# Performance work log

Hardware: AMD Instinct MI355X
Metric: run time of the kernel (lower is better)

## Reference

```python
import jax, jax.numpy as jnp
import numpy as np

T, BATCH, DMODEL, H = 2048, 16, 512, 512


def setup_inputs() -> dict:
    key = jax.random.key(0)
    ks = jax.random.split(key, 8)
    x = jax.random.normal(ks[0], (T, BATCH, DMODEL), jnp.float32)
    # initial carry: (lambda=1, h=0) so the concat trick leaves state untouched
    h0_re = jnp.zeros((1, BATCH, H), jnp.float32)
    h0_im = jnp.zeros((1, BATCH, H), jnp.float32)
    # LRU parameterization (Orvieto et al. 2023): |lambda| in [0.9, 0.99]
    u1 = jax.random.uniform(ks[1], (H,), jnp.float32)
    nu_log = jnp.log(-0.5 * jnp.log(u1 * (0.99 ** 2 - 0.9 ** 2) + 0.9 ** 2))
    theta_log = jnp.log(jax.random.uniform(ks[2], (H,), jnp.float32) * (np.pi / 10) + 1e-4)
    B_re = jax.random.normal(ks[3], (H, DMODEL), jnp.float32) / np.sqrt(2 * DMODEL)
    B_im = jax.random.normal(ks[4], (H, DMODEL), jnp.float32) / np.sqrt(2 * DMODEL)
    C_re = jax.random.normal(ks[5], (DMODEL, H), jnp.float32) / np.sqrt(H)
    C_im = jax.random.normal(ks[6], (DMODEL, H), jnp.float32) / np.sqrt(H)
    D_vec = jax.random.normal(ks[7], (DMODEL,), jnp.float32)
    return dict(x=x, h0_re=h0_re, h0_im=h0_im, nu_log=nu_log, theta_log=theta_log,
                B_re=B_re, B_im=B_im, C_re=C_re, C_im=C_im, D_vec=D_vec)


def _binop(qi, qj):
    # associative combine for h_t = a_t * h_{t-1} + b_t
    a_i, b_i = qi
    a_j, b_j = qj
    return (a_j * a_i, a_j * b_i + b_j)


def reference(x, h0_re, h0_im, nu_log, theta_log, B_re, B_im, C_re, C_im, D_vec):
    # diagonal complex recurrence eigenvalues, |Lambda| = exp(-exp(nu_log)) < 1
    Lam = jnp.exp(-jnp.exp(nu_log) + 1j * jnp.exp(theta_log))        # [H] complex64
    gamma = jnp.sqrt(1.0 - jnp.exp(-2.0 * jnp.exp(nu_log)))           # [H]
    Bmat = (B_re + 1j * B_im) * gamma[:, None]                         # [H, D]
    # map_to_h: Bu elements and broadcast Lambda elements
    Bu = jnp.einsum('tbd,hd->tbh', x.astype(jnp.complex64), Bmat)      # [T, B, H]
    Lam_el = jnp.broadcast_to(Lam, Bu.shape)                            # [T, B, H]
    # concat previous state (lambda=1, b=h0) as first scan element
    h0 = (h0_re + 1j * h0_im).astype(jnp.complex64)                    # [1, B, H]
    a = jnp.concatenate([jnp.ones_like(h0), Lam_el], axis=0)          # [T+1, B, H]
    b = jnp.concatenate([h0, Bu], axis=0)                              # [T+1, B, H]
    _, h_all = jax.lax.associative_scan(_binop, (a, b), axis=0)
    h = h_all[1:]                                                       # [T, B, H]
    # map_from_h: y = Re(C h) + D * x (elementwise skip)
    Cmat = C_re + 1j * C_im                                             # [D, H]
    y = jnp.einsum('tbh,dh->tbd', h, Cmat).real + D_vec * x            # [T, B, D]
    final_state = h[-1:]                                                # [1, B, H]
    return (final_state, y)
```

## Files before the change

kernel.cpp:

```cpp
#include <hip/hip_runtime.h>
#include <hip/hip_bf16.h>
#include <stdint.h>

typedef short shortx8 __attribute__((ext_vector_type(8)));
typedef float floatx4 __attribute__((ext_vector_type(4)));

#define T_LEN 2048
#define BATCH 16
#define DMODEL 512
#define HDIM 512
#define M_ROWS (T_LEN * BATCH)
#define NCHUNK 64
#define LCHUNK 32
#define NCHAIN (BATCH * HDIM)
#define Y_ELEMS (M_ROWS * DMODEL)

__device__ __forceinline__ unsigned short f2bf(float f) {
    union { float f; unsigned u; } v; v.f = f;
    unsigned r = (v.u + 0x7FFFu + ((v.u >> 16) & 1u)) >> 16;
    return (unsigned short)r;
}
__device__ __forceinline__ float bf2f(unsigned short u) {
    union { unsigned u; float f; } v; v.u = ((unsigned)u) << 16;
    return v.f;
}
__device__ __forceinline__ unsigned pk2(float a, float b) {
    union { __hip_bfloat162 h; unsigned u; } v;
    v.h = __float22bfloat162_rn(make_float2(a, b));
    return v.u;
}

__global__ void prep_kernel(const float* __restrict__ nu_log, const float* __restrict__ th_log,
                            float* lam_re, float* lam_im, float* l32_re, float* l32_im, float* gam) {
    int h = blockIdx.x * blockDim.x + threadIdx.x;
    if (h >= HDIM) return;
    double nu  = exp((double)nu_log[h]);
    double th  = exp((double)th_log[h]);
    double mag = exp(-nu);
    double lre = mag * cos(th), lim = mag * sin(th);
    double g   = sqrt(1.0 - exp(-2.0 * nu));
    double zr = lre, zi = lim;
    for (int i = 0; i < 5; ++i) { double nr = zr*zr - zi*zi; zi = 2.0*zr*zi; zr = nr; }
    lam_re[h] = (float)lre; lam_im[h] = (float)lim;
    l32_re[h] = (float)zr;  l32_im[h] = (float)zi;
    gam[h] = (float)g;
}

__global__ void conv_BC_kernel(const float* __restrict__ B_re, const float* __restrict__ B_im,
                               const float* __restrict__ gam,
                               const float* __restrict__ C_re, const float* __restrict__ C_im,
                               unsigned short* __restrict__ Bs, unsigned short* __restrict__ C2) {
    int idx = blockIdx.x * blockDim.x + threadIdx.x;
    if (idx < 524288) {
        int n = idx >> 9;
        int d = idx & 511;
        int h = n >> 1, pb = n & 1;
        float v = (pb ? B_im[h * DMODEL + d] : B_re[h * DMODEL + d]) * gam[h];
        Bs[idx] = f2bf(v);
    } else {
        int i2 = idx - 524288;
        int d = i2 >> 10;
        int k = i2 & 1023;
        int h = k >> 1, pb = k & 1;
        float v = pb ? -C_im[d * HDIM + h] : C_re[d * HDIM + h];
        C2[i2] = f2bf(v);
    }
}

__global__ __launch_bounds__(256, 4) void gemm_xb(const float* __restrict__ X,
                                                  const unsigned short* __restrict__ Bmat,
                                                  unsigned short* __restrict__ Out) {
    const int K = 512, N = 1024, lgNB = 3;
    __shared__ unsigned short As[128 * 64];
    __shared__ unsigned short Bsh[128 * 64];
    const int L = blockIdx.x;
    const int xcd = L & 7;
    const int slot = L >> 3;
    const int bn = slot & ((1 << lgNB) - 1);
    const int bm = xcd * 32 + (slot >> lgNB);
    const int tid = threadIdx.x;
    const int wv = tid >> 6, lane = tid & 63;
    const int wr = wv >> 1, wc = wv & 1;
    const int lrow = lane & 15, qq = lane >> 4;
    floatx4 acc[4][4] = {};

    const size_t rowA = (size_t)bm * 128, rowB = (size_t)bn * 128;
    for (int k0 = 0; k0 < K; k0 += 64) {
        #pragma unroll
        for (int j = 0; j < 4; ++j) {
            int ch  = j * 256 + wv * 64 + lane;
            int r   = ch >> 3;
            int c16 = ch & 7;
            int g16 = c16 ^ (r & 7);
            const unsigned short* gb = Bmat + (rowB + r) * (size_t)K + (k0 + g16 * 8);
            unsigned short* lb = Bsh + (size_t)(j * 256 + wv * 64) * 8;
            __builtin_amdgcn_global_load_lds((const __attribute__((address_space(1))) void*)gb,
                                             (__attribute__((address_space(3))) void*)lb, 16, 0, 0);
        }
        #pragma unroll
        for (int j = 0; j < 4; ++j) {
            int ch  = j * 256 + tid;
            int r   = ch >> 3;
            int c16 = ch & 7;
            int g16 = c16 ^ (r & 7);
            const float* gx = X + (rowA + r) * (size_t)K + (k0 + g16 * 8);
            float4 a0 = *(const float4*)gx;
            float4 a1 = *(const float4*)(gx + 4);
            uint4 w;
            w.x = pk2(a0.x, a0.y); w.y = pk2(a0.z, a0.w);
            w.z = pk2(a1.x, a1.y); w.w = pk2(a1.z, a1.w);
            *(uint4*)&As[(size_t)ch * 8] = w;
        }
        __syncthreads();
        #pragma unroll
        for (int s = 0; s < 2; ++s) {
            shortx8 af[4], bf[4];
            #pragma unroll
            for (int mi = 0; mi < 4; ++mi) {
                int row = wr * 64 + mi * 16 + lrow;
                int c16 = (s * 4 + qq) ^ (row & 7);
                af[mi] = *(const shortx8*)&As[row * 64 + c16 * 8];
            }
            #pragma unroll
            for (int ni = 0; ni < 4; ++ni) {
                int row = wc * 64 + ni * 16 + lrow;
                int c16 = (s * 4 + qq) ^ (row & 7);
                bf[ni] = *(const shortx8*)&Bsh[row * 64 + c16 * 8];
            }
            #pragma unroll
            for (int mi = 0; mi < 4; ++mi)
                #pragma unroll
                for (int ni = 0; ni < 4; ++ni)
                    acc[mi][ni] = __builtin_amdgcn_mfma_f32_16x16x32_bf16(af[mi], bf[ni], acc[mi][ni], 0, 0, 0);
        }
        __syncthreads();
    }
    #pragma unroll
    for (int mi = 0; mi < 4; ++mi) {
        int mbase = bm * 128 + wr * 64 + mi * 16 + qq * 4;
        #pragma unroll
        for (int ni = 0; ni < 4; ++ni) {
            int n = bn * 128 + wc * 64 + ni * 16 + lrow;
            #pragma unroll
            for (int r = 0; r < 4; ++r)
                Out[(size_t)(mbase + r) * N + n] = f2bf(acc[mi][ni][r]);
        }
    }
}

__global__ __launch_bounds__(256, 4) void gemm_hc(const unsigned short* __restrict__ H2,
                                                  const unsigned short* __restrict__ C2,
                                                  const float* __restrict__ X,
                                                  const float* __restrict__ Dv,
                                                  float* __restrict__ Y) {
    const int K = 1024, N = 512, lgNB = 2;
    __shared__ unsigned short As[128 * 64];
    __shared__ unsigned short Bsh[128 * 64];
    const int L = blockIdx.x;
    const int xcd = L & 7;
    const int slot = L >> 3;
    const int bn = slot & ((1 << lgNB) - 1);
    const int bm = xcd * 32 + (slot >> lgNB);
    const int tid = threadIdx.x;
    const int wv = tid >> 6, lane = tid & 63;
    const int wr = wv >> 1, wc = wv & 1;
    const int lrow = lane & 15, qq = lane >> 4;
    floatx4 acc[4][4] = {};

    const size_t rowA = (size_t)bm * 128, rowB = (size_t)bn * 128;
    for (int k0 = 0; k0 < K; k0 += 64) {
        #pragma unroll
        for (int j = 0; j < 4; ++j) {
            int ch  = j * 256 + wv * 64 + lane;
            int r   = ch >> 3;
            int c16 = ch & 7;
            int g16 = c16 ^ (r & 7);
            const unsigned short* ga = H2 + (rowA + r) * (size_t)K + (k0 + g16 * 8);
            const unsigned short* gb = C2 + (rowB + r) * (size_t)K + (k0 + g16 * 8);
            unsigned short* la = As  + (size_t)(j * 256 + wv * 64) * 8;
            unsigned short* lb = Bsh + (size_t)(j * 256 + wv * 64) * 8;
            __builtin_amdgcn_global_load_lds((const __attribute__((address_space(1))) void*)ga,
                                             (__attribute__((address_space(3))) void*)la, 16, 0, 0);
            __builtin_amdgcn_global_load_lds((const __attribute__((address_space(1))) void*)gb,
                                             (__attribute__((address_space(3))) void*)lb, 16, 0, 0);
        }
        __syncthreads();
        #pragma unroll
        for (int s = 0; s < 2; ++s) {
            shortx8 af[4], bf[4];
            #pragma unroll
            for (int mi = 0; mi < 4; ++mi) {
                int row = wr * 64 + mi * 16 + lrow;
                int c16 = (s * 4 + qq) ^ (row & 7);
                af[mi] = *(const shortx8*)&As[row * 64 + c16 * 8];
            }
            #pragma unroll
            for (int ni = 0; ni < 4; ++ni) {
                int row = wc * 64 + ni * 16 + lrow;
                int c16 = (s * 4 + qq) ^ (row & 7);
                bf[ni] = *(const shortx8*)&Bsh[row * 64 + c16 * 8];
            }
            #pragma unroll
            for (int mi = 0; mi < 4; ++mi)
                #pragma unroll
                for (int ni = 0; ni < 4; ++ni)
                    acc[mi][ni] = __builtin_amdgcn_mfma_f32_16x16x32_bf16(af[mi], bf[ni], acc[mi][ni], 0, 0, 0);
        }
        __syncthreads();
    }
    #pragma unroll
    for (int mi = 0; mi < 4; ++mi) {
        int mbase = bm * 128 + wr * 64 + mi * 16 + qq * 4;
        #pragma unroll
        for (int ni = 0; ni < 4; ++ni) {
            int n = bn * 128 + wc * 64 + ni * 16 + lrow;
            float dv = Dv[n];
            #pragma unroll
            for (int r = 0; r < 4; ++r) {
                size_t idx = (size_t)(mbase + r) * N + n;
                Y[idx] = acc[mi][ni][r] + dv * X[idx];
            }
        }
    }
}

__global__ void scan_partial(const unsigned short* __restrict__ Bu,
                             const float* __restrict__ lam_re, const float* __restrict__ lam_im,
                             float* __restrict__ car) {
    int gid = blockIdx.x * blockDim.x + threadIdx.x;
    int chunk = gid >> 11;
    int idx = gid & 2047;
    int b = idx >> 7, q = idx & 127;
    int h = q * 4;
    float4 lr4 = *(const float4*)&lam_re[h];
    float4 li4 = *(const float4*)&lam_im[h];
    float lrr[4] = {lr4.x, lr4.y, lr4.z, lr4.w};
    float lii[4] = {li4.x, li4.y, li4.z, li4.w};
    float vr[4] = {0.f, 0.f, 0.f, 0.f}, vi[4] = {0.f, 0.f, 0.f, 0.f};
    const unsigned short* p = Bu + (size_t)(chunk * LCHUNK * BATCH + b) * 1024 + q * 8;
    for (int j = 0; j < LCHUNK; ++j) {
        uint4 w = *(const uint4*)p;
        unsigned wsv[4] = {w.x, w.y, w.z, w.w};
        #pragma unroll
        for (int c = 0; c < 4; ++c) {
            float br = bf2f((unsigned short)wsv[c]);
            float bi = bf2f((unsigned short)(wsv[c] >> 16));
            float nr = lrr[c] * vr[c] - lii[c] * vi[c] + br;
            float ni = lrr[c] * vi[c] + lii[c] * vr[c] + bi;
            vr[c] = nr; vi[c] = ni;
        }
        p += BATCH * 1024;
    }
    float* cp = car + (size_t)(chunk * 2048 + idx) * 8;
    *(float4*)cp       = make_float4(vr[0], vi[0], vr[1], vi[1]);
    *(float4*)(cp + 4) = make_float4(vr[2], vi[2], vr[3], vi[3]);
}

__global__ void scan_apply(unsigned short* __restrict__ Bu,
                           const float* __restrict__ lam_re, const float* __restrict__ lam_im,
                           const float* __restrict__ l32_re, const float* __restrict__ l32_im,
                           const float* __restrict__ h0_re, const float* __restrict__ h0_im,
                           const float* __restrict__ car,
                           float* __restrict__ out_final, int interleave) {
    int gid = blockIdx.x * blockDim.x + threadIdx.x;
    int chunk = gid >> 11;
    int idx = gid & 2047;
    int b = idx >> 7, q = idx & 127;
    int h = q * 4;
    int c0 = b * 512 + h;
    float4 Lr4 = *(const float4*)&l32_re[h];
    float4 Li4 = *(const float4*)&l32_im[h];
    float Lr[4] = {Lr4.x, Lr4.y, Lr4.z, Lr4.w};
    float Li[4] = {Li4.x, Li4.y, Li4.z, Li4.w};
    float4 h0r = *(const float4*)&h0_re[c0];
    float4 h0i = *(const float4*)&h0_im[c0];
    float vr[4] = {h0r.x, h0r.y, h0r.z, h0r.w};
    float vi[4] = {h0i.x, h0i.y, h0i.z, h0i.w};
    for (int k = 0; k < chunk; ++k) {
        const float* cp = car + (size_t)(k * 2048 + idx) * 8;
        float4 a = *(const float4*)cp;
        float4 bq = *(const float4*)(cp + 4);
        float cr[4] = {a.x, a.z, bq.x, bq.z};
        float ci[4] = {a.y, a.w, bq.y, bq.w};
        #pragma unroll
        for (int c = 0; c < 4; ++c) {
            float nr = Lr[c] * vr[c] - Li[c] * vi[c] + cr[c];
            float ni = Lr[c] * vi[c] + Li[c] * vr[c] + ci[c];
            vr[c] = nr; vi[c] = ni;
        }
    }
    float4 lr4 = *(const float4*)&lam_re[h];
    float4 li4 = *(const float4*)&lam_im[h];
    float lrr[4] = {lr4.x, lr4.y, lr4.z, lr4.w};
    float lii[4] = {li4.x, li4.y, li4.z, li4.w};
    unsigned short* p = Bu + (size_t)(chunk * LCHUNK * BATCH + b) * 1024 + q * 8;
    for (int j = 0; j < LCHUNK; ++j) {
        uint4 w = *(const uint4*)p;
        unsigned wsv[4] = {w.x, w.y, w.z, w.w};
        #pragma unroll
        for (int c = 0; c < 4; ++c) {
            float br = bf2f((unsigned short)wsv[c]);
            float bi = bf2f((unsigned short)(wsv[c] >> 16));
            float nr = lrr[c] * vr[c] - lii[c] * vi[c] + br;
            float ni = lrr[c] * vi[c] + lii[c] * vr[c] + bi;
            vr[c] = nr; vi[c] = ni;
        }
        uint4 o;
        o.x = (unsigned)f2bf(vr[0]) | ((unsigned)f2bf(vi[0]) << 16);
        o.y = (unsigned)f2bf(vr[1]) | ((unsigned)f2bf(vi[1]) << 16);
        o.z = (unsigned)f2bf(vr[2]) | ((unsigned)f2bf(vi[2]) << 16);
        o.w = (unsigned)f2bf(vr[3]) | ((unsigned)f2bf(vi[3]) << 16);
        *(uint4*)p = o;
        p += BATCH * 1024;
    }
    if (chunk == NCHUNK - 1) {
        if (interleave) {
            float* o = out_final + (size_t)c0 * 2;
            *(float4*)o       = make_float4(vr[0], vi[0], vr[1], vi[1]);
            *(float4*)(o + 4) = make_float4(vr[2], vi[2], vr[3], vi[3]);
        } else {
            *(float4*)&out_final[c0] = make_float4(vr[0], vr[1], vr[2], vr[3]);
        }
    }
}

extern "C" void kernel_launch(void* const* d_in, const int* in_sizes, int n_in,
                              void* d_out, int out_size, void* d_ws, size_t ws_size,
                              hipStream_t stream) {
    const float* x        = (const float*)d_in[0];
    const float* h0_re    = (const float*)d_in[1];
    const float* h0_im    = (const float*)d_in[2];
    const float* nu_log   = (const float*)d_in[3];
    const float* theta_lg = (const float*)d_in[4];
    const float* B_re     = (const float*)d_in[5];
    const float* B_im     = (const float*)d_in[6];
    const float* C_re     = (const float*)d_in[7];
    const float* C_im     = (const float*)d_in[8];
    const float* D_vec    = (const float*)d_in[9];

    char* ws = (char*)d_ws;
    unsigned short* BuH  = (unsigned short*)(ws + 0);
    unsigned short* Bs   = (unsigned short*)(ws + 67108864);
    unsigned short* C2   = (unsigned short*)(ws + 68157440);
    float* car           = (float*)(ws + 69206016);
    float* lam_re        = (float*)(ws + 73400320);
    float* lam_im        = (float*)(ws + 73402368);
    float* l32_re        = (float*)(ws + 73404416);
    float* l32_im        = (float*)(ws + 73406464);
    float* gam           = (float*)(ws + 73408512);

    int fs_elems = out_size - Y_ELEMS;
    int interleave = (fs_elems == 8192) ? 0 : 1;
    if (fs_elems != 8192) fs_elems = 16384;
    float* out_final = (float*)d_out;
    float* y_out     = (float*)d_out + fs_elems;

    prep_kernel<<<2, 256, 0, stream>>>(nu_log, theta_lg, lam_re, lam_im, l32_re, l32_im, gam);
    conv_BC_kernel<<<4096, 256, 0, stream>>>(B_re, B_im, gam, C_re, C_im, Bs, C2);
    gemm_xb<<<2048, 256, 0, stream>>>(x, Bs, BuH);
    scan_partial<<<512, 256, 0, stream>>>(BuH, lam_re, lam_im, car);
    scan_apply<<<512, 256, 0, stream>>>(BuH, lam_re, lam_im, l32_re, l32_im,
                                        h0_re, h0_im, car, out_final, interleave);
    gemm_hc<<<1024, 256, 0, stream>>>(BuH, C2, x, D_vec, y_out);
}
```

Baseline: 279.3 us.

## Pre-cast x to bf16 and use 256-row tiles with async LDS loads in input GEMM

Adds a separate kernel that converts x to bf16 once. The input projection GEMM now loads A tiles with global_load_lds and uses 256x128 tiles, which halves the grid and doubles per-block M reuse. The output GEMM reads the bf16 copy of x for the D skip term, so that term loses precision. The gamma computation moves from prep_kernel into conv_BC, and an extra pass over x plus a 32 MB workspace buffer are added.

```diff
diff --git a/kernel.cpp b/kernel.cpp
--- a/kernel.cpp
+++ b/kernel.cpp
@@ -24,30 +24,23 @@
     union { unsigned u; float f; } v; v.u = ((unsigned)u) << 16;
     return v.f;
 }
-__device__ __forceinline__ unsigned pk2(float a, float b) {
-    union { __hip_bfloat162 h; unsigned u; } v;
-    v.h = __float22bfloat162_rn(make_float2(a, b));
-    return v.u;
-}
 
 __global__ void prep_kernel(const float* __restrict__ nu_log, const float* __restrict__ th_log,
-                            float* lam_re, float* lam_im, float* l32_re, float* l32_im, float* gam) {
+                            float* lam_re, float* lam_im, float* l32_re, float* l32_im) {
     int h = blockIdx.x * blockDim.x + threadIdx.x;
     if (h >= HDIM) return;
     double nu  = exp((double)nu_log[h]);
     double th  = exp((double)th_log[h]);
     double mag = exp(-nu);
     double lre = mag * cos(th), lim = mag * sin(th);
-    double g   = sqrt(1.0 - exp(-2.0 * nu));
     double zr = lre, zi = lim;
     for (int i = 0; i < 5; ++i) { double nr = zr*zr - zi*zi; zi = 2.0*zr*zi; zr = nr; }
     lam_re[h] = (float)lre; lam_im[h] = (float)lim;
     l32_re[h] = (float)zr;  l32_im[h] = (float)zi;
-    gam[h] = (float)g;
 }
 
 __global__ void conv_BC_kernel(const float* __restrict__ B_re, const float* __restrict__ B_im,
-                               const float* __restrict__ gam,
+                               const float* __restrict__ nu_log,
                                const float* __restrict__ C_re, const float* __restrict__ C_im,
                                unsigned short* __restrict__ Bs, unsigned short* __restrict__ C2) {
     int idx = blockIdx.x * blockDim.x + threadIdx.x;
@@ -55,7 +48,8 @@
         int n = idx >> 9;
         int d = idx & 511;
         int h = n >> 1, pb = n & 1;
-        float v = (pb ? B_im[h * DMODEL + d] : B_re[h * DMODEL + d]) * gam[h];
+        float g = sqrtf(1.0f - expf(-2.0f * expf(nu_log[h])));
+        float v = (pb ? B_im[h * DMODEL + d] : B_re[h * DMODEL + d]) * g;
         Bs[idx] = f2bf(v);
     } else {
         int i2 = idx - 524288;
@@ -67,25 +61,45 @@
     }
 }
 
-__global__ __launch_bounds__(256, 4) void gemm_xb(const float* __restrict__ X,
+__global__ void cast_x_kernel(const float4* __restrict__ x4, unsigned short* __restrict__ xb, int n4) {
+    int i = blockIdx.x * blockDim.x + threadIdx.x;
+    if (i >= n4) return;
+    float4 v = x4[i];
+    ushort4 u;
+    u.x = f2bf(v.x); u.y = f2bf(v.y); u.z = f2bf(v.z); u.w = f2bf(v.w);
+    *(ushort4*)(xb + (size_t)i * 4) = u;
+}
+
+__global__ __launch_bounds__(256) void gemm_xb256(const unsigned short* __restrict__ A,
                                                   const unsigned short* __restrict__ Bmat,
                                                   unsigned short* __restrict__ Out) {
-    const int K = 512, N = 1024, lgNB = 3;
-    __shared__ unsigned short As[128 * 64];
+    const int K = 512, N = 1024;
+    __shared__ unsigned short As[256 * 64];
     __shared__ unsigned short Bsh[128 * 64];
     const int L = blockIdx.x;
     const int xcd = L & 7;
     const int slot = L >> 3;
-    const int bn = slot & ((1 << lgNB) - 1);
-    const int bm = xcd * 32 + (slot >> lgNB);
+    const int bn = slot & 7;
+    const int bm = xcd * 16 + (slot >> 3);
     const int tid = threadIdx.x;
     const int wv = tid >> 6, lane = tid & 63;
     const int wr = wv >> 1, wc = wv & 1;
     const int lrow = lane & 15, qq = lane >> 4;
-    floatx4 acc[4][4] = {};
-
-    const size_t rowA = (size_t)bm * 128, rowB = (size_t)bn * 128;
+    floatx4 acc[8][4] = {};
+
+    const size_t rowA = (size_t)bm * 256, rowB = (size_t)bn * 128;
     for (int k0 = 0; k0 < K; k0 += 64) {
+        #pragma unroll
+        for (int j = 0; j < 8; ++j) {
+            int ch  = j * 256 + wv * 64 + lane;
+            int r   = ch >> 3;
+            int c16 = ch & 7;
+            int g16 = c16 ^ (r & 7);
+            const unsigned short* ga = A + (rowA + r) * (size_t)K + (k0 + g16 * 8);
+            unsigned short* la = As + (size_t)(j * 256 + wv * 64) * 8;
+            __builtin_amdgcn_global_load_lds((const __attribute__((address_space(1))) void*)ga,
+                                             (__attribute__((address_space(3))) void*)la, 16, 0, 0);
+        }
         #pragma unroll
         for (int j = 0; j < 4; ++j) {
             int ch  = j * 256 + wv * 64 + lane;
@@ -97,27 +111,13 @@
             __builtin_amdgcn_global_load_lds((const __attribute__((address_space(1))) void*)gb,
                                              (__attribute__((address_space(3))) void*)lb, 16, 0, 0);
         }
-        #pragma unroll
-        for (int j = 0; j < 4; ++j) {
-            int ch  = j * 256 + tid;
-            int r   = ch >> 3;
-            int c16 = ch & 7;
-            int g16 = c16 ^ (r & 7);
-            const float* gx = X + (rowA + r) * (size_t)K + (k0 + g16 * 8);
-            float4 a0 = *(const float4*)gx;
-            float4 a1 = *(const float4*)(gx + 4);
-            uint4 w;
-            w.x = pk2(a0.x, a0.y); w.y = pk2(a0.z, a0.w);
-            w.z = pk2(a1.x, a1.y); w.w = pk2(a1.z, a1.w);
-            *(uint4*)&As[(size_t)ch * 8] = w;
-        }
         __syncthreads();
         #pragma unroll
         for (int s = 0; s < 2; ++s) {
-            shortx8 af[4], bf[4];
-            #pragma unroll
-            for (int mi = 0; mi < 4; ++mi) {
-                int row = wr * 64 + mi * 16 + lrow;
+            shortx8 af[8], bf[4];
+            #pragma unroll
+            for (int mi = 0; mi < 8; ++mi) {
+                int row = wr * 128 + mi * 16 + lrow;
                 int c16 = (s * 4 + qq) ^ (row & 7);
                 af[mi] = *(const shortx8*)&As[row * 64 + c16 * 8];
             }
@@ -128,7 +128,7 @@
                 bf[ni] = *(const shortx8*)&Bsh[row * 64 + c16 * 8];
             }
             #pragma unroll
-            for (int mi = 0; mi < 4; ++mi)
+            for (int mi = 0; mi < 8; ++mi)
                 #pragma unroll
                 for (int ni = 0; ni < 4; ++ni)
                     acc[mi][ni] = __builtin_amdgcn_mfma_f32_16x16x32_bf16(af[mi], bf[ni], acc[mi][ni], 0, 0, 0);
@@ -136,8 +136,8 @@
         __syncthreads();
     }
     #pragma unroll
-    for (int mi = 0; mi < 4; ++mi) {
-        int mbase = bm * 128 + wr * 64 + mi * 16 + qq * 4;
+    for (int mi = 0; mi < 8; ++mi) {
+        int mbase = bm * 256 + wr * 128 + mi * 16 + qq * 4;
         #pragma unroll
         for (int ni = 0; ni < 4; ++ni) {
             int n = bn * 128 + wc * 64 + ni * 16 + lrow;
@@ -150,7 +150,7 @@
 
 __global__ __launch_bounds__(256, 4) void gemm_hc(const unsigned short* __restrict__ H2,
                                                   const unsigned short* __restrict__ C2,
-                                                  const float* __restrict__ X,
+                                                  const unsigned short* __restrict__ Xb,
                                                   const float* __restrict__ Dv,
                                                   float* __restrict__ Y) {
     const int K = 1024, N = 512, lgNB = 2;
@@ -218,7 +218,7 @@
             #pragma unroll
             for (int r = 0; r < 4; ++r) {
                 size_t idx = (size_t)(mbase + r) * N + n;
-                Y[idx] = acc[mi][ni][r] + dv * X[idx];
+                Y[idx] = acc[mi][ni][r] + dv * bf2f(Xb[idx]);
             }
         }
     }
@@ -340,14 +340,14 @@
 
     char* ws = (char*)d_ws;
     unsigned short* BuH  = (unsigned short*)(ws + 0);
-    unsigned short* Bs   = (unsigned short*)(ws + 67108864);
-    unsigned short* C2   = (unsigned short*)(ws + 68157440);
-    float* car           = (float*)(ws + 69206016);
-    float* lam_re        = (float*)(ws + 73400320);
-    float* lam_im        = (float*)(ws + 73402368);
-    float* l32_re        = (float*)(ws + 73404416);
-    float* l32_im        = (float*)(ws + 73406464);
-    float* gam           = (float*)(ws + 73408512);
+    unsigned short* xb   = (unsigned short*)(ws + 67108864);
+    unsigned short* Bs   = (unsigned short*)(ws + 100663296);
+    unsigned short* C2   = (unsigned short*)(ws + 101711872);
+    float* car           = (float*)(ws + 102760448);
+    float* lam_re        = (float*)(ws + 106954752);
+    float* lam_im        = (float*)(ws + 106956800);
+    float* l32_re        = (float*)(ws + 106958848);
+    float* l32_im        = (float*)(ws + 106960896);
 
     int fs_elems = out_size - Y_ELEMS;
     int interleave = (fs_elems == 8192) ? 0 : 1;
@@ -355,11 +355,12 @@
     float* out_final = (float*)d_out;
     float* y_out     = (float*)d_out + fs_elems;
 
-    prep_kernel<<<2, 256, 0, stream>>>(nu_log, theta_lg, lam_re, lam_im, l32_re, l32_im, gam);
-    conv_BC_kernel<<<4096, 256, 0, stream>>>(B_re, B_im, gam, C_re, C_im, Bs, C2);
-    gemm_xb<<<2048, 256, 0, stream>>>(x, Bs, BuH);
+    prep_kernel<<<2, 256, 0, stream>>>(nu_log, theta_lg, lam_re, lam_im, l32_re, l32_im);
+    conv_BC_kernel<<<4096, 256, 0, stream>>>(B_re, B_im, nu_log, C_re, C_im, Bs, C2);
+    cast_x_kernel<<<(Y_ELEMS / 4) / 256, 256, 0, stream>>>((const float4*)x, xb, Y_ELEMS / 4);
+    gemm_xb256<<<1024, 256, 0, stream>>>(xb, Bs, BuH);
     scan_partial<<<512, 256, 0, stream>>>(BuH, lam_re, lam_im, car);
     scan_apply<<<512, 256, 0, stream>>>(BuH, lam_re, lam_im, l32_re, l32_im,
                                         h0_re, h0_im, car, out_final, interleave);
-    gemm_hc<<<1024, 256, 0, stream>>>(BuH, C2, x, D_vec, y_out);
-}
+    gemm_hc<<<1024, 256, 0, stream>>>(BuH, C2, xb, D_vec, y_out);
+}
```

Result: slower. 295.8 us (+5.9%).
